# Kernel tuning notes

Measured on AMD Instinct MI355X. Metric: run time of the kernel, lower is better.

The kernel has to match this reference:

```python
import jax, jax.numpy as jnp
import numpy as np

N, E, B = 50000, 800000, 64
IN, H, OUT = 64, 128, 64


def _gcn_norm(edge_index, num_nodes):
    # PyG gcn_norm with add_self_loops=True: A_hat = A + I, norm = d^-1/2[src]*d^-1/2[dst]
    loop = jnp.arange(num_nodes)
    src = jnp.concatenate([edge_index[0], loop])
    dst = jnp.concatenate([edge_index[1], loop])
    deg = jax.ops.segment_sum(jnp.ones_like(dst, dtype=jnp.float32), dst,
                              num_segments=num_nodes)  # >= 1 due to self-loops
    dis = deg ** -0.5
    norm = dis[src] * dis[dst]  # [E+N]
    return src, dst, norm


def _gcn_layer(x, W, b, src, dst, norm, num_nodes):
    h = x @ W                                   # linear first (GCNConv order)
    msg = h[src] * norm[:, None]                # gather + normalize, [E+N, H]
    out = jax.ops.segment_sum(msg, dst, num_segments=num_nodes)  # scatter-add
    return out + b


def setup_inputs() -> dict:
    key = jax.random.key(0)
    ks = jax.random.split(key, 12)
    x = jax.random.normal(ks[0], (N, IN), dtype=jnp.float32)
    edge_index = jax.random.randint(ks[1], (2, E), 0, N, dtype=jnp.int64)
    batch = jnp.sort(jax.random.randint(ks[2], (N,), 0, B, dtype=jnp.int64))

    def lin(k, fan_in, fan_out):
        s = 1.0 / np.sqrt(fan_in)
        return jax.random.uniform(k, (fan_in, fan_out), jnp.float32, -s, s)

    return {
        "x": x, "edge_index": edge_index, "batch": batch,
        "W1": lin(ks[3], IN, H), "b1": jnp.zeros((H,), jnp.float32),
        "W2": lin(ks[4], H, H),  "b2": jnp.zeros((H,), jnp.float32),
        "W3": lin(ks[5], H, H),  "b3": jnp.zeros((H,), jnp.float32),
        "W4": lin(ks[6], H, OUT), "b4": jnp.zeros((OUT,), jnp.float32),
    }


def reference(x, edge_index, batch, W1, b1, W2, b2, W3, b3, W4, b4):
    src, dst, norm = _gcn_norm(edge_index, N)
    h = jax.nn.relu(_gcn_layer(x, W1, b1, src, dst, norm, N))
    h = jax.nn.relu(_gcn_layer(h, W2, b2, src, dst, norm, N))
    # global mean pool over graphs
    sums = jax.ops.segment_sum(h, batch, num_segments=B)          # [B, H]
    cnts = jax.ops.segment_sum(jnp.ones((N,), jnp.float32), batch, num_segments=B)
    pooled = sums / jnp.maximum(cnts, 1.0)[:, None]
    # MLP head
    return jax.nn.relu(pooled @ W3 + b3) @ W4 + b4                # [B, OUT]
```

## Files before the change

kernel.cpp:

```cpp
#include <hip/hip_runtime.h>


__device__ __forceinline__ float ldf(const void* p, long long i, int f32) {
    if (f32) return ((const float*)p)[i];
    unsigned int u = ((const unsigned short*)p)[i];
    return __uint_as_float(u << 16);
}
__device__ __forceinline__ float bfl(unsigned int u) { return __uint_as_float(u << 16); }
__device__ __forceinline__ float bfh(unsigned int u) { return __uint_as_float(u & 0xFFFF0000u); }
__device__ __forceinline__ int ld_idx(const int* p, long long i, int i64) {
    return i64 ? p[2 * i] : p[i];
}
__device__ __forceinline__ unsigned short f2bf(float v) {
    unsigned int x = __float_as_uint(v);
    return (unsigned short)((x + 0x7FFFu + ((x >> 16) & 1u)) >> 16);
}
__device__ __forceinline__ int clampi(int v, int lo, int hi) {
    return v < lo ? lo : (v > hi ? hi : v);
}

#define OW1 0
#define OB1 8192
#define OW2 8320
#define OB2 24704
// ... 1 lines not shown
#define OB3 41216
#define OW4 41344
#define OB4 49536
#define OTOT 49600


__global__ void gnn_prep(const void* W1, const void* b1, const void* W2, const void* b2,
                         const void* W3, const void* b3, const void* W4, const void* b4,
                         const void* x, const int* __restrict__ ei,
                         int* __restrict__ flags_out,
                         int* __restrict__ degcnt, float* __restrict__ pooled,
                         float* __restrict__ wsW, unsigned short* __restrict__ xb,
                         int N, int B) {
    __shared__ int s_cnt, s_or;
    const int t = threadIdx.x;
    if (t == 0) { s_cnt = 0; s_or = 0; }
    __syncthreads();
    {
        const unsigned int* w1w = (const unsigned int*)W1;
        int c = 0, o = 0;
        for (int i = t; i < 512; i += 256) {
            unsigned int e = (w1w[i] >> 7) & 0xFFu;
            if (e >= 100 && e <= 140) c++;
        }
        for (int i = t; i < 1024; i += 256) o |= ei[2 * i + 1];
        atomicAdd(&s_cnt, c);
        atomicOr(&s_or, o);
    }
    __syncthreads();
    const int f32 = (s_cnt > 256) ? 0 : 1;
    if (blockIdx.x == 0 && t == 0) {
        flags_out[0] = f32;
        flags_out[1] = (s_or == 0) ? 1 : 0;
    }
    const int i = blockIdx.x * 256 + t;
    const int stride = gridDim.x * 256;
    for (int j = i; j < N; j += stride) degcnt[j] = 0;
    for (int j = i; j < B * 128; j += stride) pooled[j] = 0.f;
    for (int j = i; j < OTOT; j += stride) {
        float v;
        if      (j < OB1) v = ldf(W1, j - OW1, f32);
        else if (j < OW2) v = ldf(b1, j - OB1, f32);
        else if (j < OB2) v = ldf(W2, j - OW2, f32);
        else if (j < OW3) v = ldf(b2, j - OB2, f32);
        else if (j < OB3) v = ldf(W3, j - OW3, f32);
        else if (j < OW4) v = ldf(b3, j - OB3, f32);
        else if (j < OB4) v = ldf(W4, j - OW4, f32);
        else              v = ldf(b4, j - OB4, f32);
        wsW[j] = v;
    }
    if (f32) {
        const float* xf = (const float*)x;
        for (int j = i; j < N * 64; j += stride) xb[j] = f2bf(xf[j]);
    }
}


__global__ void gnn_hist(const int* __restrict__ ei, int E, int N,
                         const int* __restrict__ flags, int* __restrict__ degcnt,
                         int* __restrict__ rank) {
    int base = (blockIdx.x * 256 + threadIdx.x) * 4;
    if (base >= E) return;
    int i64 = flags[1];
    int m = min(4, E - base);
    int d[4], r[4];
#pragma unroll
    for (int j = 0; j < 4; ++j)
        if (j < m) d[j] = clampi(ld_idx(ei, (long long)E + base + j, i64), 0, N - 1);
#pragma unroll
    for (int j = 0; j < 4; ++j)
        if (j < m) r[j] = atomicAdd(&degcnt[d[j]], 1);
#pragma unroll
    for (int j = 0; j < 4; ++j)
        if (j < m) rank[base + j] = r[j];
}

__global__ void gnn_scan1(const int* __restrict__ cnt, int* __restrict__ excl,
                          int* __restrict__ sums, float* __restrict__ dis, int N) {
    __shared__ int sh[256];
    int t = threadIdx.x;
    int i = blockIdx.x * 256 + t;
    int v = (i < N) ? cnt[i] : 0;
    sh[t] = v;
    __syncthreads();
    for (int off = 1; off < 256; off <<= 1) {
        int a = (t >= off) ? sh[t - off] : 0;
        __syncthreads();
        sh[t] += a;
        __syncthreads();
    }
    if (i < N) {
        excl[i] = sh[t] - v;
        dis[i] = rsqrtf((float)v + 1.0f);
    }
    if (t == 255) sums[blockIdx.x] = sh[255];
}

__global__ void gnn_scan2(int* __restrict__ sums, int nb) {
    __shared__ int sh[256];
    int t = threadIdx.x;
    int v = (t < nb) ? sums[t] : 0;
    sh[t] = v;
    __syncthreads();
    for (int off = 1; off < 256; off <<= 1) {
        int a = (t >= off) ? sh[t - off] : 0;
        __syncthreads();
        sh[t] += a;
        __syncthreads();
    }
    if (t < nb) sums[t] = sh[t] - v;
}

template <bool SMALLN>
__global__ void gnn_fill(const int* __restrict__ ei, const int* __restrict__ excl,
                         const int* __restrict__ bsums, const int* __restrict__ rank,
                         void* __restrict__ csr, int E, int N,
                         const int* __restrict__ flags) {
    int e = blockIdx.x * 256 + threadIdx.x;
    if (e >= E) return;
    int i64 = flags[1];
    int s = clampi(ld_idx(ei, (long long)e, i64), 0, N - 1);
    int d = clampi(ld_idx(ei, (long long)E + e, i64), 0, N - 1);
    int pos = excl[d] + bsums[d >> 8] + rank[e];
    if (SMALLN) ((unsigned short*)csr)[pos] = (unsigned short)s;
    else        ((int*)csr)[pos] = s;
}

template <bool SMALLN>
__device__ __forceinline__ int csr_at(const void* csr, int e) {
    return SMALLN ? (int)((const unsigned short*)csr)[e] : ((const int*)csr)[e];
}


template <bool SMALLN>
__global__ __launch_bounds__(128) void gnn_aggx_lin1(const void* __restrict__ x,
                                                     const unsigned short* __restrict__ xconv,
                                                     const int* __restrict__ excl,
                                                     const int* __restrict__ bsums,
                                                     const void* __restrict__ csr,
                                                     const float* __restrict__ dis,
                                                     const int* __restrict__ flags,
                                                     const float* __restrict__ Wf,
                                                     const float* __restrict__ bias,
                                                     int N, int E, float* __restrict__ out) {
    __shared__ float Xs[16 * 64];
    const unsigned int* tab = flags[0] ? (const unsigned int*)xconv : (const unsigned int*)x;
    const int t = threadIdx.x;
    const int nbase = blockIdx.x * 16;
    const int lane = t & 63;
    const int fl = lane & 31;

#pragma unroll
    for (int pass = 0; pass < 4; ++pass) {
        int ln = pass * 4 + (t >> 6) * 2 + (lane >> 5);
        int n = nbase + ln;
        float a0 = 0.f, a1 = 0.f;
        if (n < N) {
            float dn = dis[n], dn2 = dn * dn;
            unsigned int us = tab[(long long)n * 32 + fl];
            a0 = bfl(us) * dn2; a1 = bfh(us) * dn2;
            int beg = excl[n] + bsums[n >> 8];
            int end = (n + 1 < N) ? (excl[n + 1] + bsums[(n + 1) >> 8]) : E;
            int e = beg;
            for (; e + 8 <= end; e += 8) {
                int s0 = csr_at<SMALLN>(csr, e),     s1 = csr_at<SMALLN>(csr, e + 1);
                int s2 = csr_at<SMALLN>(csr, e + 2), s3 = csr_at<SMALLN>(csr, e + 3);
                int s4 = csr_at<SMALLN>(csr, e + 4), s5 = csr_at<SMALLN>(csr, e + 5);
                int s6 = csr_at<SMALLN>(csr, e + 6), s7 = csr_at<SMALLN>(csr, e + 7);
                float w0 = dis[s0], w1 = dis[s1], w2 = dis[s2], w3 = dis[s3];
                float w4 = dis[s4], w5 = dis[s5], w6 = dis[s6], w7 = dis[s7];
                unsigned int u0 = tab[(long long)s0 * 32 + fl];
                unsigned int u1 = tab[(long long)s1 * 32 + fl];
                unsigned int u2 = tab[(long long)s2 * 32 + fl];
                unsigned int u3 = tab[(long long)s3 * 32 + fl];
                unsigned int u4 = tab[(long long)s4 * 32 + fl];
                unsigned int u5 = tab[(long long)s5 * 32 + fl];
                unsigned int u6 = tab[(long long)s6 * 32 + fl];
// ... 36 lines not shown
    __syncthreads();

    const int fg = t & 31, ng = t >> 5;
    const int f0 = fg * 4, n0 = ng * 4;
    const float4* Xs4 = (const float4*)Xs;
    const float4* Wp  = (const float4*)Wf;
    float4 acc[4];
#pragma unroll
    for (int j = 0; j < 4; ++j) acc[j] = make_float4(0.f, 0.f, 0.f, 0.f);
#pragma unroll 4
    for (int k4 = 0; k4 < 16; ++k4) {
        const float4 wa = Wp[(4 * k4 + 0) * 32 + fg];
        const float4 wb = Wp[(4 * k4 + 1) * 32 + fg];
        const float4 wc = Wp[(4 * k4 + 2) * 32 + fg];
        const float4 wd = Wp[(4 * k4 + 3) * 32 + fg];
#pragma unroll
        for (int j = 0; j < 4; ++j) {
            const float4 xv = Xs4[(n0 + j) * 16 + k4];
            acc[j].x = fmaf(xv.x, wa.x, acc[j].x); acc[j].y = fmaf(xv.x, wa.y, acc[j].y);
            acc[j].z = fmaf(xv.x, wa.z, acc[j].z); acc[j].w = fmaf(xv.x, wa.w, acc[j].w);
            acc[j].x = fmaf(xv.y, wb.x, acc[j].x); acc[j].y = fmaf(xv.y, wb.y, acc[j].y);
            acc[j].z = fmaf(xv.y, wb.z, acc[j].z); acc[j].w = fmaf(xv.y, wb.w, acc[j].w);
            acc[j].x = fmaf(xv.z, wc.x, acc[j].x); acc[j].y = fmaf(xv.z, wc.y, acc[j].y);
            acc[j].z = fmaf(xv.z, wc.z, acc[j].z); acc[j].w = fmaf(xv.z, wc.w, acc[j].w);
            acc[j].x = fmaf(xv.w, wd.x, acc[j].x); acc[j].y = fmaf(xv.w, wd.y, acc[j].y);
            acc[j].z = fmaf(xv.w, wd.z, acc[j].z); acc[j].w = fmaf(xv.w, wd.w, acc[j].w);
        }
    }
    const float4 b = *(const float4*)&bias[f0];
#pragma unroll
    for (int j = 0; j < 4; ++j) {
        int n = nbase + n0 + j;
        if (n >= N) continue;
        float4 a = acc[j];
        a.x = fmaxf(a.x + b.x, 0.f);
        a.y = fmaxf(a.y + b.y, 0.f);
        a.z = fmaxf(a.z + b.z, 0.f);
        a.w = fmaxf(a.w + b.w, 0.f);
        *(float4*)(out + (long long)n * 128 + f0) = a;
    }
}


template <int K, bool RELU, bool OUTBF>
__global__ __launch_bounds__(128) void gnn_linear(const float* __restrict__ X,
                                                  const float* __restrict__ Wf,
                                                  const float* __restrict__ bias,
                                                  int N, void* __restrict__ out) {
    __shared__ float Xs[16 * K];
    const int t = threadIdx.x;
    const int nbase = blockIdx.x * 16;

#pragma unroll
    for (int it = 0; it < K / 32; ++it) {
        int i4 = t + it * 128;
        int n = nbase + (i4 * 4) / K;
        float4 v = make_float4(0.f, 0.f, 0.f, 0.f);
        if (n < N) v = ((const float4*)X)[(long long)nbase * (K / 4) + i4];
        ((float4*)Xs)[i4] = v;
    }
    __syncthreads();

    const int fg = t & 31, ng = t >> 5;
    const int f0 = fg * 4, n0 = ng * 4;
    const float4* Xs4 = (const float4*)Xs;
    const float4* Wp  = (const float4*)Wf;
    float4 acc[4];
#pragma unroll
    for (int j = 0; j < 4; ++j) acc[j] = make_float4(0.f, 0.f, 0.f, 0.f);
#pragma unroll 4
    for (int k4 = 0; k4 < K / 4; ++k4) {
        const float4 wa = Wp[(4 * k4 + 0) * 32 + fg];
        const float4 wb = Wp[(4 * k4 + 1) * 32 + fg];
        const float4 wc = Wp[(4 * k4 + 2) * 32 + fg];
        const float4 wd = Wp[(4 * k4 + 3) * 32 + fg];
#pragma unroll
        for (int j = 0; j < 4; ++j) {
            const float4 xv = Xs4[(n0 + j) * (K / 4) + k4];
            acc[j].x = fmaf(xv.x, wa.x, acc[j].x); acc[j].y = fmaf(xv.x, wa.y, acc[j].y);
            acc[j].z = fmaf(xv.x, wa.z, acc[j].z); acc[j].w = fmaf(xv.x, wa.w, acc[j].w);
            acc[j].x = fmaf(xv.y, wb.x, acc[j].x); acc[j].y = fmaf(xv.y, wb.y, acc[j].y);
            acc[j].z = fmaf(xv.y, wb.z, acc[j].z); acc[j].w = fmaf(xv.y, wb.w, acc[j].w);
            acc[j].x = fmaf(xv.z, wc.x, acc[j].x); acc[j].y = fmaf(xv.z, wc.y, acc[j].y);
            acc[j].z = fmaf(xv.z, wc.z, acc[j].z); acc[j].w = fmaf(xv.z, wc.w, acc[j].w);
            acc[j].x = fmaf(xv.w, wd.x, acc[j].x); acc[j].y = fmaf(xv.w, wd.y, acc[j].y);
            acc[j].z = fmaf(xv.w, wd.z, acc[j].z); acc[j].w = fmaf(xv.w, wd.w, acc[j].w);
        }
    }
#pragma unroll
    for (int j = 0; j < 4; ++j) {
        int n = nbase + n0 + j;
        if (n >= N) continue;
        float4 a = acc[j];
        if (RELU) {
            const float4 b = *(const float4*)&bias[f0];
            a.x = fmaxf(a.x + b.x, 0.f);
            a.y = fmaxf(a.y + b.y, 0.f);
            a.z = fmaxf(a.z + b.z, 0.f);
            a.w = fmaxf(a.w + b.w, 0.f);
        }
        if (OUTBF) {
            uint2 u;
            u.x = (unsigned int)f2bf(a.x) | ((unsigned int)f2bf(a.y) << 16);
            u.y = (unsigned int)f2bf(a.z) | ((unsigned int)f2bf(a.w) << 16);
            *(uint2*)((unsigned short*)out + (long long)n * 128 + f0) = u;
        } else {
            *(float4*)((float*)out + (long long)n * 128 + f0) = a;
        }
    }
}


template <bool SMALLN>
__global__ __launch_bounds__(256) void gnn_agg_bf(const unsigned short* __restrict__ A2,
                                                  const int* __restrict__ excl,
                                                  const int* __restrict__ bsums,
                                                  const void* __restrict__ csr,
                                                  const float* __restrict__ dis,
                                                  const float* __restrict__ bias,
                                                  float* __restrict__ outC, int N, int E) {
    int t = threadIdx.x;
    int lane = t & 63;
    int n = blockIdx.x * 8 + (t >> 6) * 2 + (lane >> 5);
    if (n >= N) return;
    int fl = lane & 31;
    float dn = dis[n];
    float dn2 = dn * dn;
    uint2 us = *(const uint2*)(A2 + (long long)n * 128 + fl * 4);
    float a0 = bfl(us.x) * dn2, a1 = bfh(us.x) * dn2;
    float a2 = bfl(us.y) * dn2, a3 = bfh(us.y) * dn2;
    int beg = excl[n] + bsums[n >> 8];
    int end = (n + 1 < N) ? (excl[n + 1] + bsums[(n + 1) >> 8]) : E;
    int e = beg;
    for (; e + 8 <= end; e += 8) {
        int s0 = csr_at<SMALLN>(csr, e),     s1 = csr_at<SMALLN>(csr, e + 1);
        int s2 = csr_at<SMALLN>(csr, e + 2), s3 = csr_at<SMALLN>(csr, e + 3);
        int s4 = csr_at<SMALLN>(csr, e + 4), s5 = csr_at<SMALLN>(csr, e + 5);
        int s6 = csr_at<SMALLN>(csr, e + 6), s7 = csr_at<SMALLN>(csr, e + 7);
        float w0 = dis[s0], w1 = dis[s1], w2 = dis[s2], w3 = dis[s3];
        float w4 = dis[s4], w5 = dis[s5], w6 = dis[s6], w7 = dis[s7];
        uint2 u0 = *(const uint2*)(A2 + (long long)s0 * 128 + fl * 4);
        uint2 u1 = *(const uint2*)(A2 + (long long)s1 * 128 + fl * 4);
        uint2 u2 = *(const uint2*)(A2 + (long long)s2 * 128 + fl * 4);
        uint2 u3 = *(const uint2*)(A2 + (long long)s3 * 128 + fl * 4);
        uint2 u4 = *(const uint2*)(A2 + (long long)s4 * 128 + fl * 4);
        uint2 u5 = *(const uint2*)(A2 + (long long)s5 * 128 + fl * 4);
        uint2 u6 = *(const uint2*)(A2 + (long long)s6 * 128 + fl * 4);
        uint2 u7 = *(const uint2*)(A2 + (long long)s7 * 128 + fl * 4);
        w0 *= dn; w1 *= dn; w2 *= dn; w3 *= dn;
        w4 *= dn; w5 *= dn; w6 *= dn; w7 *= dn;
        a0 = fmaf(w0, bfl(u0.x), a0); a1 = fmaf(w0, bfh(u0.x), a1);
        a2 = fmaf(w0, bfl(u0.y), a2); a3 = fmaf(w0, bfh(u0.y), a3);
        a0 = fmaf(w1, bfl(u1.x), a0); a1 = fmaf(w1, bfh(u1.x), a1);
        a2 = fmaf(w1, bfl(u1.y), a2); a3 = fmaf(w1, bfh(u1.y), a3);
        a0 = fmaf(w2, bfl(u2.x), a0); a1 = fmaf(w2, bfh(u2.x), a1);
        a2 = fmaf(w2, bfl(u2.y), a2); a3 = fmaf(w2, bfh(u2.y), a3);
        a0 = fmaf(w3, bfl(u3.x), a0); a1 = fmaf(w3, bfh(u3.x), a1);
        a2 = fmaf(w3, bfl(u3.y), a2); a3 = fmaf(w3, bfh(u3.y), a3);
        a0 = fmaf(w4, bfl(u4.x), a0); a1 = fmaf(w4, bfh(u4.x), a1);
        a2 = fmaf(w4, bfl(u4.y), a2); a3 = fmaf(w4, bfh(u4.y), a3);
        a0 = fmaf(w5, bfl(u5.x), a0); a1 = fmaf(w5, bfh(u5.x), a1);
        a2 = fmaf(w5, bfl(u5.y), a2); a3 = fmaf(w5, bfh(u5.y), a3);
        a0 = fmaf(w6, bfl(u6.x), a0); a1 = fmaf(w6, bfh(u6.x), a1);
        a2 = fmaf(w6, bfl(u6.y), a2); a3 = fmaf(w6, bfh(u6.y), a3);
        a0 = fmaf(w7, bfl(u7.x), a0); a1 = fmaf(w7, bfh(u7.x), a1);
        a2 = fmaf(w7, bfl(u7.y), a2); a3 = fmaf(w7, bfh(u7.y), a3);
    }
    for (; e + 4 <= end; e += 4) {
        int s0 = csr_at<SMALLN>(csr, e),     s1 = csr_at<SMALLN>(csr, e + 1);
        int s2 = csr_at<SMALLN>(csr, e + 2), s3 = csr_at<SMALLN>(csr, e + 3);
        float w0 = dis[s0], w1 = dis[s1], w2 = dis[s2], w3 = dis[s3];
        uint2 u0 = *(const uint2*)(A2 + (long long)s0 * 128 + fl * 4);
        uint2 u1 = *(const uint2*)(A2 + (long long)s1 * 128 + fl * 4);
        uint2 u2 = *(const uint2*)(A2 + (long long)s2 * 128 + fl * 4);
        uint2 u3 = *(const uint2*)(A2 + (long long)s3 * 128 + fl * 4);
        w0 *= dn; w1 *= dn; w2 *= dn; w3 *= dn;
        a0 = fmaf(w0, bfl(u0.x), a0); a1 = fmaf(w0, bfh(u0.x), a1);
        a2 = fmaf(w0, bfl(u0.y), a2); a3 = fmaf(w0, bfh(u0.y), a3);
        a0 = fmaf(w1, bfl(u1.x), a0); a1 = fmaf(w1, bfh(u1.x), a1);
        a2 = fmaf(w1, bfl(u1.y), a2); a3 = fmaf(w1, bfh(u1.y), a3);
        a0 = fmaf(w2, bfl(u2.x), a0); a1 = fmaf(w2, bfh(u2.x), a1);
        a2 = fmaf(w2, bfl(u2.y), a2); a3 = fmaf(w2, bfh(u2.y), a3);
        a0 = fmaf(w3, bfl(u3.x), a0); a1 = fmaf(w3, bfh(u3.x), a1);
        a2 = fmaf(w3, bfl(u3.y), a2); a3 = fmaf(w3, bfh(u3.y), a3);
    }
    for (; e < end; ++e) {
        int s = csr_at<SMALLN>(csr, e);
        float w = dis[s] * dn;
        uint2 u = *(const uint2*)(A2 + (long long)s * 128 + fl * 4);
        a0 = fmaf(w, bfl(u.x), a0); a1 = fmaf(w, bfh(u.x), a1);
        a2 = fmaf(w, bfl(u.y), a2); a3 = fmaf(w, bfh(u.y), a3);
    }
    const float4 b = *(const float4*)&bias[fl * 4];
    float4 o;
    o.x = fmaxf(a0 + b.x, 0.f);
    o.y = fmaxf(a1 + b.y, 0.f);
    o.z = fmaxf(a2 + b.z, 0.f);
    o.w = fmaxf(a3 + b.w, 0.f);
    *(float4*)(outC + (long long)n * 128 + fl * 4) = o;
}


#define PSTRIP 32
__global__ __launch_bounds__(128) void gnn_pool(const float* __restrict__ h,
                                                const int* __restrict__ batch,
                                                const int* __restrict__ flags,
                                                float* __restrict__ pooled, int N, int B) {
    int i64 = flags[1];
    int f = threadIdx.x;
    int n0 = blockIdx.x * PSTRIP;
    if (n0 >= N) return;
    int nend = min(n0 + PSTRIP, N);
    int cur = clampi(ld_idx(batch, n0, i64), 0, B - 1);
    float acc = 0.0f;
    for (int n = n0; n < nend; ++n) {
        int b = clampi(ld_idx(batch, n, i64), 0, B - 1);
        if (b != cur) {
            atomicAdd(&pooled[cur * 128 + f], acc);
            acc = 0.0f; cur = b;
        }
        acc += h[(long long)n * 128 + f];
    }
    atomicAdd(&pooled[cur * 128 + f], acc);
}


__global__ __launch_bounds__(128) void gnn_head(const float* __restrict__ pooled,
                                                const int* __restrict__ batch,
                                                const float* __restrict__ W3,
                                                const float* __restrict__ b3,
                                                const float* __restrict__ W4,
                                                const float* __restrict__ b4,
// ... 17 lines not shown
    __syncthreads();
    float acc = b3[f];
    for (int k = 0; k < 128; ++k) acc = fmaf(xs[k], W3[k * 128 + f], acc);
    rs[f] = fmaxf(acc, 0.f);
    __syncthreads();
    if (f < 64) {
        float a2 = b4[f];
        for (int k = 0; k < 128; ++k) a2 = fmaf(rs[k], W4[k * 64 + f], a2);
        if (flags[0]) ((float*)outv)[b * 64 + f] = a2;
        else          ((unsigned short*)outv)[b * 64 + f] = f2bf(a2);
    }
}


extern "C" void kernel_launch(void* const* d_in, const int* in_sizes, int n_in,
                              void* d_out, int out_size, void* d_ws, size_t ws_size,
                              hipStream_t stream) {
    const void* x  = d_in[0];
    const int* ei  = (const int*)d_in[1];
    const int* bat = (const int*)d_in[2];

    const int N = in_sizes[0] / 64;
    const int E = in_sizes[1] / 2;
    const int B = out_size / 64;
    const bool smalln = (N < 65536);

    char* p = (char*)d_ws;
    auto alloc = [&](size_t bytes) { void* q = (void*)p; p += (bytes + 255) & ~(size_t)255; return q; };
    int*   flags    = (int*)alloc(256);
    float* wsW      = (float*)alloc((size_t)OTOT * 4);
    int*   degcnt   = (int*)alloc((size_t)N * 4);
    float* dis      = (float*)alloc((size_t)N * 4);
    int*   excl     = (int*)alloc((size_t)N * 4);
    int*   bsums    = (int*)alloc(1024);
    int*   rank     = (int*)alloc((size_t)E * 4);
    void*  csr      = alloc((size_t)E * (smalln ? 2 : 4));
    unsigned short* xb = (unsigned short*)alloc((size_t)N * 64 * 2);
    float* H1       = (float*)alloc((size_t)N * 128 * 4);
    float* C2       = (float*)alloc((size_t)N * 128 * 4);
    unsigned short* A2 = (unsigned short*)alloc((size_t)N * 128 * 2);
    float* pooled   = (float*)alloc((size_t)B * 128 * 4);
    (void)ws_size; (void)n_in;

    const int nbN = (N + 255) / 256;

    gnn_prep<<<512, 256, 0, stream>>>(d_in[3], d_in[4], d_in[5], d_in[6],
                                      d_in[7], d_in[8], d_in[9], d_in[10],
                                      x, ei, flags, degcnt, pooled, wsW, xb, N, B);

    gnn_hist<<<(E + 1023) / 1024, 256, 0, stream>>>(ei, E, N, flags, degcnt, rank);
    gnn_scan1<<<nbN, 256, 0, stream>>>(degcnt, excl, bsums, dis, N);
    gnn_scan2<<<1, 256, 0, stream>>>(bsums, nbN);
    if (smalln)
        gnn_fill<true><<<(E + 255) / 256, 256, 0, stream>>>(ei, excl, bsums, rank, csr, E, N, flags);
    else
        gnn_fill<false><<<(E + 255) / 256, 256, 0, stream>>>(ei, excl, bsums, rank, csr, E, N, flags);

    const int nlin = (N + 15) / 16;
    const int nagg = (N + 7) / 8;

    if (smalln)
        gnn_aggx_lin1<true><<<nlin, 128, 0, stream>>>(x, xb, excl, bsums, csr, dis, flags,
                                                      wsW + OW1, wsW + OB1, N, E, H1);
    else
        gnn_aggx_lin1<false><<<nlin, 128, 0, stream>>>(x, xb, excl, bsums, csr, dis, flags,
                                                       wsW + OW1, wsW + OB1, N, E, H1);

    gnn_linear<128, false, true><<<nlin, 128, 0, stream>>>(H1, wsW + OW2, wsW + OB2, N, (void*)A2);
    if (smalln)
        gnn_agg_bf<true><<<nagg, 256, 0, stream>>>(A2, excl, bsums, csr, dis, wsW + OB2, C2, N, E);
    else
        gnn_agg_bf<false><<<nagg, 256, 0, stream>>>(A2, excl, bsums, csr, dis, wsW + OB2, C2, N, E);

    gnn_pool<<<(N + PSTRIP - 1) / PSTRIP, 128, 0, stream>>>(C2, bat, flags, pooled, N, B);
    gnn_head<<<B, 128, 0, stream>>>(pooled, bat, wsW + OW3, wsW + OB3,
                                    wsW + OW4, wsW + OB4, flags, d_out, N);
}
```

Baseline: 272.2 us.

## Fuse layer-2 aggregation with linear and merge scan passes via last-block pattern

Layer 2 now aggregates first on bf16 H1 (stored by the layer-1 kernel in bf16) and then applies W2 in the same kernel. This removes the separate linear kernel and the fp32 H1 round trip. The two-kernel scan is merged into one using an atomic done-counter so the last block computes the block offsets, saving a launch. The cost is that layer 2 now gathers 128-wide bf16 rows from a reordered aggregate-then-transform schedule, and H1 is quantized to bf16.

```diff
diff --git a/kernel.cpp b/kernel.cpp
--- a/kernel.cpp
+++ b/kernel.cpp
@@ -57,6 +57,7 @@
     if (blockIdx.x == 0 && t == 0) {
         flags_out[0] = f32;
         flags_out[1] = (s_or == 0) ? 1 : 0;
+        flags_out[8] = 0;
     }
     const int i = blockIdx.x * 256 + t;
     const int stride = gridDim.x * 256;
@@ -101,8 +102,11 @@
 }
 
 __global__ void gnn_scan1(const int* __restrict__ cnt, int* __restrict__ excl,
-                          int* __restrict__ sums, float* __restrict__ dis, int N) {
+                          int* __restrict__ sums, int* __restrict__ bsums,
+                          float* __restrict__ dis, int* __restrict__ done,
+                          int N, int nb) {
     __shared__ int sh[256];
+    __shared__ int isLast;
     int t = threadIdx.x;
     int i = blockIdx.x * 256 + t;
     int v = (i < N) ? cnt[i] : 0;
@@ -119,13 +123,13 @@
         dis[i] = rsqrtf((float)v + 1.0f);
     }
     if (t == 255) sums[blockIdx.x] = sh[255];
-}
-
-__global__ void gnn_scan2(int* __restrict__ sums, int nb) {
-    __shared__ int sh[256];
-    int t = threadIdx.x;
-    int v = (t < nb) ? sums[t] : 0;
-    sh[t] = v;
+    __threadfence();
+    __syncthreads();
+    if (t == 0) isLast = (atomicAdd(done, 1) == nb - 1) ? 1 : 0;
+    __syncthreads();
+    if (!isLast) return;
+    int v2 = (t < nb) ? sums[t] : 0;
+    sh[t] = v2;
     __syncthreads();
     for (int off = 1; off < 256; off <<= 1) {
         int a = (t >= off) ? sh[t - off] : 0;
@@ -133,7 +137,7 @@
         sh[t] += a;
         __syncthreads();
     }
-    if (t < nb) sums[t] = sh[t] - v;
+    if (t < nb) bsums[t] = sh[t] - v2;
 }
 
 template <bool SMALLN>
@@ -167,7 +171,8 @@
                                                      const int* __restrict__ flags,
                                                      const float* __restrict__ Wf,
                                                      const float* __restrict__ bias,
-                                                     int N, int E, float* __restrict__ out) {
+                                                     int N, int E,
+                                                     unsigned short* __restrict__ out) {
     __shared__ float Xs[16 * 64];
     const unsigned int* tab = flags[0] ? (const unsigned int*)xconv : (const unsigned int*)x;
     const int t = threadIdx.x;
@@ -270,32 +275,107 @@
     for (int j = 0; j < 4; ++j) {
         int n = nbase + n0 + j;
         if (n >= N) continue;
-        float4 a = acc[j];
-        a.x = fmaxf(a.x + b.x, 0.f);
-        a.y = fmaxf(a.y + b.y, 0.f);
-        a.z = fmaxf(a.z + b.z, 0.f);
-        a.w = fmaxf(a.w + b.w, 0.f);
-        *(float4*)(out + (long long)n * 128 + f0) = a;
-    }
-}
-
-
-template <int K, bool RELU, bool OUTBF>
-__global__ __launch_bounds__(128) void gnn_linear(const float* __restrict__ X,
-                                                  const float* __restrict__ Wf,
-                                                  const float* __restrict__ bias,
-                                                  int N, void* __restrict__ out) {
-    __shared__ float Xs[16 * K];
+        float ax = fmaxf(acc[j].x + b.x, 0.f);
+        float ay = fmaxf(acc[j].y + b.y, 0.f);
+        float az = fmaxf(acc[j].z + b.z, 0.f);
+        float aw = fmaxf(acc[j].w + b.w, 0.f);
+        uint2 u;
+        u.x = (unsigned int)f2bf(ax) | ((unsigned int)f2bf(ay) << 16);
+        u.y = (unsigned int)f2bf(az) | ((unsigned int)f2bf(aw) << 16);
+        *(uint2*)(out + (long long)n * 128 + f0) = u;
+    }
+}
+
+
+template <bool SMALLN>
+__global__ __launch_bounds__(128) void gnn_agg_lin2(const unsigned short* __restrict__ H1,
+                                                    const int* __restrict__ excl,
+                                                    const int* __restrict__ bsums,
+                                                    const void* __restrict__ csr,
+                                                    const float* __restrict__ dis,
+                                                    const float* __restrict__ Wf,
+                                                    const float* __restrict__ bias,
+                                                    int N, int E, float* __restrict__ outC) {
+    __shared__ float Xs[16 * 128];
     const int t = threadIdx.x;
     const int nbase = blockIdx.x * 16;
-
-#pragma unroll
-    for (int it = 0; it < K / 32; ++it) {
-        int i4 = t + it * 128;
-        int n = nbase + (i4 * 4) / K;
-        float4 v = make_float4(0.f, 0.f, 0.f, 0.f);
-        if (n < N) v = ((const float4*)X)[(long long)nbase * (K / 4) + i4];
-        ((float4*)Xs)[i4] = v;
+    const int lane = t & 63;
+    const int fl = lane & 31;
+
+#pragma unroll
+    for (int pass = 0; pass < 4; ++pass) {
+        int ln = pass * 4 + (t >> 6) * 2 + (lane >> 5);
+        int n = nbase + ln;
+        float a0 = 0.f, a1 = 0.f, a2 = 0.f, a3 = 0.f;
+        if (n < N) {
+            float dn = dis[n], dn2 = dn * dn;
+            uint2 us = *(const uint2*)(H1 + (long long)n * 128 + fl * 4);
+            a0 = bfl(us.x) * dn2; a1 = bfh(us.x) * dn2;
+            a2 = bfl(us.y) * dn2; a3 = bfh(us.y) * dn2;
+            int beg = excl[n] + bsums[n >> 8];
+            int end = (n + 1 < N) ? (excl[n + 1] + bsums[(n + 1) >> 8]) : E;
+            int e = beg;
+            for (; e + 8 <= end; e += 8) {
+                int s0 = csr_at<SMALLN>(csr, e),     s1 = csr_at<SMALLN>(csr, e + 1);
+                int s2 = csr_at<SMALLN>(csr, e + 2), s3 = csr_at<SMALLN>(csr, e + 3);
+                int s4 = csr_at<SMALLN>(csr, e + 4), s5 = csr_at<SMALLN>(csr, e + 5);
+                int s6 = csr_at<SMALLN>(csr, e + 6), s7 = csr_at<SMALLN>(csr, e + 7);
+                float w0 = dis[s0], w1 = dis[s1], w2 = dis[s2], w3 = dis[s3];
+                float w4 = dis[s4], w5 = dis[s5], w6 = dis[s6], w7 = dis[s7];
+                uint2 u0 = *(const uint2*)(H1 + (long long)s0 * 128 + fl * 4);
+                uint2 u1 = *(const uint2*)(H1 + (long long)s1 * 128 + fl * 4);
+                uint2 u2 = *(const uint2*)(H1 + (long long)s2 * 128 + fl * 4);
+                uint2 u3 = *(const uint2*)(H1 + (long long)s3 * 128 + fl * 4);
+                uint2 u4 = *(const uint2*)(H1 + (long long)s4 * 128 + fl * 4);
+                uint2 u5 = *(const uint2*)(H1 + (long long)s5 * 128 + fl * 4);
+                uint2 u6 = *(const uint2*)(H1 + (long long)s6 * 128 + fl * 4);
+                uint2 u7 = *(const uint2*)(H1 + (long long)s7 * 128 + fl * 4);
+                w0 *= dn; w1 *= dn; w2 *= dn; w3 *= dn;
+                w4 *= dn; w5 *= dn; w6 *= dn; w7 *= dn;
+                a0 = fmaf(w0, bfl(u0.x), a0); a1 = fmaf(w0, bfh(u0.x), a1);
+                a2 = fmaf(w0, bfl(u0.y), a2); a3 = fmaf(w0, bfh(u0.y), a3);
+                a0 = fmaf(w1, bfl(u1.x), a0); a1 = fmaf(w1, bfh(u1.x), a1);
+                a2 = fmaf(w1, bfl(u1.y), a2); a3 = fmaf(w1, bfh(u1.y), a3);
+                a0 = fmaf(w2, bfl(u2.x), a0); a1 = fmaf(w2, bfh(u2.x), a1);
+                a2 = fmaf(w2, bfl(u2.y), a2); a3 = fmaf(w2, bfh(u2.y), a3);
+                a0 = fmaf(w3, bfl(u3.x), a0); a1 = fmaf(w3, bfh(u3.x), a1);
+                a2 = fmaf(w3, bfl(u3.y), a2); a3 = fmaf(w3, bfh(u3.y), a3);
+                a0 = fmaf(w4, bfl(u4.x), a0); a1 = fmaf(w4, bfh(u4.x), a1);
+                a2 = fmaf(w4, bfl(u4.y), a2); a3 = fmaf(w4, bfh(u4.y), a3);
+                a0 = fmaf(w5, bfl(u5.x), a0); a1 = fmaf(w5, bfh(u5.x), a1);
+                a2 = fmaf(w5, bfl(u5.y), a2); a3 = fmaf(w5, bfh(u5.y), a3);
+                a0 = fmaf(w6, bfl(u6.x), a0); a1 = fmaf(w6, bfh(u6.x), a1);
+                a2 = fmaf(w6, bfl(u6.y), a2); a3 = fmaf(w6, bfh(u6.y), a3);
+                a0 = fmaf(w7, bfl(u7.x), a0); a1 = fmaf(w7, bfh(u7.x), a1);
+                a2 = fmaf(w7, bfl(u7.y), a2); a3 = fmaf(w7, bfh(u7.y), a3);
+            }
+            for (; e + 4 <= end; e += 4) {
+                int s0 = csr_at<SMALLN>(csr, e),     s1 = csr_at<SMALLN>(csr, e + 1);
+                int s2 = csr_at<SMALLN>(csr, e + 2), s3 = csr_at<SMALLN>(csr, e + 3);
+                float w0 = dis[s0], w1 = dis[s1], w2 = dis[s2], w3 = dis[s3];
+                uint2 u0 = *(const uint2*)(H1 + (long long)s0 * 128 + fl * 4);
+                uint2 u1 = *(const uint2*)(H1 + (long long)s1 * 128 + fl * 4);
+                uint2 u2 = *(const uint2*)(H1 + (long long)s2 * 128 + fl * 4);
+                uint2 u3 = *(const uint2*)(H1 + (long long)s3 * 128 + fl * 4);
+                w0 *= dn; w1 *= dn; w2 *= dn; w3 *= dn;
+                a0 = fmaf(w0, bfl(u0.x), a0); a1 = fmaf(w0, bfh(u0.x), a1);
+                a2 = fmaf(w0, bfl(u0.y), a2); a3 = fmaf(w0, bfh(u0.y), a3);
+                a0 = fmaf(w1, bfl(u1.x), a0); a1 = fmaf(w1, bfh(u1.x), a1);
+                a2 = fmaf(w1, bfl(u1.y), a2); a3 = fmaf(w1, bfh(u1.y), a3);
+                a0 = fmaf(w2, bfl(u2.x), a0); a1 = fmaf(w2, bfh(u2.x), a1);
+                a2 = fmaf(w2, bfl(u2.y), a2); a3 = fmaf(w2, bfh(u2.y), a3);
+                a0 = fmaf(w3, bfl(u3.x), a0); a1 = fmaf(w3, bfh(u3.x), a1);
+                a2 = fmaf(w3, bfl(u3.y), a2); a3 = fmaf(w3, bfh(u3.y), a3);
+            }
+            for (; e < end; ++e) {
+                int s = csr_at<SMALLN>(csr, e);
+                float w = dis[s] * dn;
+                uint2 u = *(const uint2*)(H1 + (long long)s * 128 + fl * 4);
+                a0 = fmaf(w, bfl(u.x), a0); a1 = fmaf(w, bfh(u.x), a1);
+                a2 = fmaf(w, bfl(u.y), a2); a3 = fmaf(w, bfh(u.y), a3);
+            }
+        }
+        *(float4*)&Xs[ln * 128 + fl * 4] = make_float4(a0, a1, a2, a3);
     }
     __syncthreads();
 
@@ -307,14 +387,14 @@
 #pragma unroll
     for (int j = 0; j < 4; ++j) acc[j] = make_float4(0.f, 0.f, 0.f, 0.f);
 #pragma unroll 4
-    for (int k4 = 0; k4 < K / 4; ++k4) {
+    for (int k4 = 0; k4 < 32; ++k4) {
         const float4 wa = Wp[(4 * k4 + 0) * 32 + fg];
         const float4 wb = Wp[(4 * k4 + 1) * 32 + fg];
         const float4 wc = Wp[(4 * k4 + 2) * 32 + fg];
         const float4 wd = Wp[(4 * k4 + 3) * 32 + fg];
 #pragma unroll
         for (int j = 0; j < 4; ++j) {
-            const float4 xv = Xs4[(n0 + j) * (K / 4) + k4];
+            const float4 xv = Xs4[(n0 + j) * 32 + k4];
             acc[j].x = fmaf(xv.x, wa.x, acc[j].x); acc[j].y = fmaf(xv.x, wa.y, acc[j].y);
             acc[j].z = fmaf(xv.x, wa.z, acc[j].z); acc[j].w = fmaf(xv.x, wa.w, acc[j].w);
             acc[j].x = fmaf(xv.y, wb.x, acc[j].x); acc[j].y = fmaf(xv.y, wb.y, acc[j].y);
@@ -325,117 +405,18 @@
             acc[j].z = fmaf(xv.w, wd.z, acc[j].z); acc[j].w = fmaf(xv.w, wd.w, acc[j].w);
         }
     }
+    const float4 b = *(const float4*)&bias[f0];
 #pragma unroll
     for (int j = 0; j < 4; ++j) {
         int n = nbase + n0 + j;
         if (n >= N) continue;
         float4 a = acc[j];
-        if (RELU) {
-            const float4 b = *(const float4*)&bias[f0];
-            a.x = fmaxf(a.x + b.x, 0.f);
-            a.y = fmaxf(a.y + b.y, 0.f);
-            a.z = fmaxf(a.z + b.z, 0.f);
-            a.w = fmaxf(a.w + b.w, 0.f);
-        }
-        if (OUTBF) {
-            uint2 u;
-            u.x = (unsigned int)f2bf(a.x) | ((unsigned int)f2bf(a.y) << 16);
-            u.y = (unsigned int)f2bf(a.z) | ((unsigned int)f2bf(a.w) << 16);
-            *(uint2*)((unsigned short*)out + (long long)n * 128 + f0) = u;
-        } else {
-            *(float4*)((float*)out + (long long)n * 128 + f0) = a;
-        }
-    }
-}
-
-
-template <bool SMALLN>
-__global__ __launch_bounds__(256) void gnn_agg_bf(const unsigned short* __restrict__ A2,
-                                                  const int* __restrict__ excl,
-                                                  const int* __restrict__ bsums,
-                                                  const void* __restrict__ csr,
-                                                  const float* __restrict__ dis,
-                                                  const float* __restrict__ bias,
-                                                  float* __restrict__ outC, int N, int E) {
-    int t = threadIdx.x;
-    int lane = t & 63;
-    int n = blockIdx.x * 8 + (t >> 6) * 2 + (lane >> 5);
-    if (n >= N) return;
-    int fl = lane & 31;
-    float dn = dis[n];
-    float dn2 = dn * dn;
-    uint2 us = *(const uint2*)(A2 + (long long)n * 128 + fl * 4);
-    float a0 = bfl(us.x) * dn2, a1 = bfh(us.x) * dn2;
-    float a2 = bfl(us.y) * dn2, a3 = bfh(us.y) * dn2;
-    int beg = excl[n] + bsums[n >> 8];
-    int end = (n + 1 < N) ? (excl[n + 1] + bsums[(n + 1) >> 8]) : E;
-    int e = beg;
-    for (; e + 8 <= end; e += 8) {
-        int s0 = csr_at<SMALLN>(csr, e),     s1 = csr_at<SMALLN>(csr, e + 1);
-        int s2 = csr_at<SMALLN>(csr, e + 2), s3 = csr_at<SMALLN>(csr, e + 3);
-        int s4 = csr_at<SMALLN>(csr, e + 4), s5 = csr_at<SMALLN>(csr, e + 5);
-        int s6 = csr_at<SMALLN>(csr, e + 6), s7 = csr_at<SMALLN>(csr, e + 7);
-        float w0 = dis[s0], w1 = dis[s1], w2 = dis[s2], w3 = dis[s3];
-        float w4 = dis[s4], w5 = dis[s5], w6 = dis[s6], w7 = dis[s7];
-        uint2 u0 = *(const uint2*)(A2 + (long long)s0 * 128 + fl * 4);
-        uint2 u1 = *(const uint2*)(A2 + (long long)s1 * 128 + fl * 4);
-        uint2 u2 = *(const uint2*)(A2 + (long long)s2 * 128 + fl * 4);
-        uint2 u3 = *(const uint2*)(A2 + (long long)s3 * 128 + fl * 4);
-        uint2 u4 = *(const uint2*)(A2 + (long long)s4 * 128 + fl * 4);
-        uint2 u5 = *(const uint2*)(A2 + (long long)s5 * 128 + fl * 4);
-        uint2 u6 = *(const uint2*)(A2 + (long long)s6 * 128 + fl * 4);
-        uint2 u7 = *(const uint2*)(A2 + (long long)s7 * 128 + fl * 4);
-        w0 *= dn; w1 *= dn; w2 *= dn; w3 *= dn;
-        w4 *= dn; w5 *= dn; w6 *= dn; w7 *= dn;
-        a0 = fmaf(w0, bfl(u0.x), a0); a1 = fmaf(w0, bfh(u0.x), a1);
-        a2 = fmaf(w0, bfl(u0.y), a2); a3 = fmaf(w0, bfh(u0.y), a3);
-        a0 = fmaf(w1, bfl(u1.x), a0); a1 = fmaf(w1, bfh(u1.x), a1);
-        a2 = fmaf(w1, bfl(u1.y), a2); a3 = fmaf(w1, bfh(u1.y), a3);
-        a0 = fmaf(w2, bfl(u2.x), a0); a1 = fmaf(w2, bfh(u2.x), a1);
-        a2 = fmaf(w2, bfl(u2.y), a2); a3 = fmaf(w2, bfh(u2.y), a3);
-        a0 = fmaf(w3, bfl(u3.x), a0); a1 = fmaf(w3, bfh(u3.x), a1);
-        a2 = fmaf(w3, bfl(u3.y), a2); a3 = fmaf(w3, bfh(u3.y), a3);
-        a0 = fmaf(w4, bfl(u4.x), a0); a1 = fmaf(w4, bfh(u4.x), a1);
-        a2 = fmaf(w4, bfl(u4.y), a2); a3 = fmaf(w4, bfh(u4.y), a3);
-        a0 = fmaf(w5, bfl(u5.x), a0); a1 = fmaf(w5, bfh(u5.x), a1);
-        a2 = fmaf(w5, bfl(u5.y), a2); a3 = fmaf(w5, bfh(u5.y), a3);
-        a0 = fmaf(w6, bfl(u6.x), a0); a1 = fmaf(w6, bfh(u6.x), a1);
-        a2 = fmaf(w6, bfl(u6.y), a2); a3 = fmaf(w6, bfh(u6.y), a3);
-        a0 = fmaf(w7, bfl(u7.x), a0); a1 = fmaf(w7, bfh(u7.x), a1);
-        a2 = fmaf(w7, bfl(u7.y), a2); a3 = fmaf(w7, bfh(u7.y), a3);
-    }
-    for (; e + 4 <= end; e += 4) {
-        int s0 = csr_at<SMALLN>(csr, e),     s1 = csr_at<SMALLN>(csr, e + 1);
-        int s2 = csr_at<SMALLN>(csr, e + 2), s3 = csr_at<SMALLN>(csr, e + 3);
-        float w0 = dis[s0], w1 = dis[s1], w2 = dis[s2], w3 = dis[s3];
-        uint2 u0 = *(const uint2*)(A2 + (long long)s0 * 128 + fl * 4);
-        uint2 u1 = *(const uint2*)(A2 + (long long)s1 * 128 + fl * 4);
-        uint2 u2 = *(const uint2*)(A2 + (long long)s2 * 128 + fl * 4);
-        uint2 u3 = *(const uint2*)(A2 + (long long)s3 * 128 + fl * 4);
-        w0 *= dn; w1 *= dn; w2 *= dn; w3 *= dn;
-        a0 = fmaf(w0, bfl(u0.x), a0); a1 = fmaf(w0, bfh(u0.x), a1);
-        a2 = fmaf(w0, bfl(u0.y), a2); a3 = fmaf(w0, bfh(u0.y), a3);
-        a0 = fmaf(w1, bfl(u1.x), a0); a1 = fmaf(w1, bfh(u1.x), a1);
-        a2 = fmaf(w1, bfl(u1.y), a2); a3 = fmaf(w1, bfh(u1.y), a3);
-        a0 = fmaf(w2, bfl(u2.x), a0); a1 = fmaf(w2, bfh(u2.x), a1);
-        a2 = fmaf(w2, bfl(u2.y), a2); a3 = fmaf(w2, bfh(u2.y), a3);
-        a0 = fmaf(w3, bfl(u3.x), a0); a1 = fmaf(w3, bfh(u3.x), a1);
-        a2 = fmaf(w3, bfl(u3.y), a2); a3 = fmaf(w3, bfh(u3.y), a3);
-    }
-    for (; e < end; ++e) {
-        int s = csr_at<SMALLN>(csr, e);
-        float w = dis[s] * dn;
-        uint2 u = *(const uint2*)(A2 + (long long)s * 128 + fl * 4);
-        a0 = fmaf(w, bfl(u.x), a0); a1 = fmaf(w, bfh(u.x), a1);
-        a2 = fmaf(w, bfl(u.y), a2); a3 = fmaf(w, bfh(u.y), a3);
-    }
-    const float4 b = *(const float4*)&bias[fl * 4];
-    float4 o;
-    o.x = fmaxf(a0 + b.x, 0.f);
-    o.y = fmaxf(a1 + b.y, 0.f);
-    o.z = fmaxf(a2 + b.z, 0.f);
-    o.w = fmaxf(a3 + b.w, 0.f);
-    *(float4*)(outC + (long long)n * 128 + fl * 4) = o;
+        a.x = fmaxf(a.x + b.x, 0.f);
+        a.y = fmaxf(a.y + b.y, 0.f);
+        a.z = fmaxf(a.z + b.z, 0.f);
+        a.w = fmaxf(a.w + b.w, 0.f);
+        *(float4*)(outC + (long long)n * 128 + f0) = a;
+    }
 }
 
 
@@ -519,13 +500,13 @@
     int*   degcnt   = (int*)alloc((size_t)N * 4);
     float* dis      = (float*)alloc((size_t)N * 4);
     int*   excl     = (int*)alloc((size_t)N * 4);
+    int*   sums     = (int*)alloc(1024);
     int*   bsums    = (int*)alloc(1024);
     int*   rank     = (int*)alloc((size_t)E * 4);
     void*  csr      = alloc((size_t)E * (smalln ? 2 : 4));
     unsigned short* xb = (unsigned short*)alloc((size_t)N * 64 * 2);
-    float* H1       = (float*)alloc((size_t)N * 128 * 4);
+    unsigned short* H1 = (unsigned short*)alloc((size_t)N * 128 * 2);
     float* C2       = (float*)alloc((size_t)N * 128 * 4);
-    unsigned short* A2 = (unsigned short*)alloc((size_t)N * 128 * 2);
     float* pooled   = (float*)alloc((size_t)B * 128 * 4);
     (void)ws_size; (void)n_in;
 
@@ -536,15 +517,13 @@
                                       x, ei, flags, degcnt, pooled, wsW, xb, N, B);
 
     gnn_hist<<<(E + 1023) / 1024, 256, 0, stream>>>(ei, E, N, flags, degcnt, rank);
-    gnn_scan1<<<nbN, 256, 0, stream>>>(degcnt, excl, bsums, dis, N);
-    gnn_scan2<<<1, 256, 0, stream>>>(bsums, nbN);
+    gnn_scan1<<<nbN, 256, 0, stream>>>(degcnt, excl, sums, bsums, dis, flags + 8, N, nbN);
     if (smalln)
         gnn_fill<true><<<(E + 255) / 256, 256, 0, stream>>>(ei, excl, bsums, rank, csr, E, N, flags);
     else
         gnn_fill<false><<<(E + 255) / 256, 256, 0, stream>>>(ei, excl, bsums, rank, csr, E, N, flags);
 
     const int nlin = (N + 15) / 16;
-    const int nagg = (N + 7) / 8;
 
     if (smalln)
         gnn_aggx_lin1<true><<<nlin, 128, 0, stream>>>(x, xb, excl, bsums, csr, dis, flags,
@@ -553,11 +532,12 @@
         gnn_aggx_lin1<false><<<nlin, 128, 0, stream>>>(x, xb, excl, bsums, csr, dis, flags,
                                                        wsW + OW1, wsW + OB1, N, E, H1);
 
-    gnn_linear<128, false, true><<<nlin, 128, 0, stream>>>(H1, wsW + OW2, wsW + OB2, N, (void*)A2);
     if (smalln)
-        gnn_agg_bf<true><<<nagg, 256, 0, stream>>>(A2, excl, bsums, csr, dis, wsW + OB2, C2, N, E);
+        gnn_agg_lin2<true><<<nlin, 128, 0, stream>>>(H1, excl, bsums, csr, dis,
+                                                     wsW + OW2, wsW + OB2, N, E, C2);
     else
-        gnn_agg_bf<false><<<nagg, 256, 0, stream>>>(A2, excl, bsums, csr, dis, wsW + OB2, C2, N, E);
+        gnn_agg_lin2<false><<<nlin, 128, 0, stream>>>(H1, excl, bsums, csr, dis,
+                                                      wsW + OW2, wsW + OB2, N, E, C2);
 
     gnn_pool<<<(N + PSTRIP - 1) / PSTRIP, 128, 0, stream>>>(C2, bat, flags, pooled, N, B);
     gnn_head<<<B, 128, 0, stream>>>(pooled, bat, wsW + OW3, wsW + OB3,
```

After: 276.5 us. No clear change (+1.6%).

## Split layer-2 aggregation into feature quarters and fuse scan passes

Applied to the files above, without the earlier changes.

The layer-2 aggregation kernel now has each 16-thread group handle one quarter of a node's 128 features with 4-byte loads. Blocks are ordered so the four quarter-blocks of the same node group are adjacent, which is meant to improve cache locality and spread the gather across more threads. Separately, the two-kernel block-sum scan is merged into one kernel: the last block to finish, found with an atomic counter, scans the block sums, removing one launch. The cost is four times as many CSR index and dis reads per edge, plus a threadfence and atomic in the scan.

```diff
diff --git a/kernel.cpp b/kernel.cpp
--- a/kernel.cpp
+++ b/kernel.cpp
@@ -57,6 +57,7 @@
     if (blockIdx.x == 0 && t == 0) {
         flags_out[0] = f32;
         flags_out[1] = (s_or == 0) ? 1 : 0;
+        flags_out[8] = 0;
     }
     const int i = blockIdx.x * 256 + t;
     const int stride = gridDim.x * 256;
@@ -101,8 +102,11 @@
 }
 
 __global__ void gnn_scan1(const int* __restrict__ cnt, int* __restrict__ excl,
-                          int* __restrict__ sums, float* __restrict__ dis, int N) {
+                          int* __restrict__ sums, int* __restrict__ bsums,
+                          float* __restrict__ dis, int* __restrict__ done,
+                          int N, int nb) {
     __shared__ int sh[256];
+    __shared__ int isLast;
     int t = threadIdx.x;
     int i = blockIdx.x * 256 + t;
     int v = (i < N) ? cnt[i] : 0;
@@ -119,13 +123,13 @@
         dis[i] = rsqrtf((float)v + 1.0f);
     }
     if (t == 255) sums[blockIdx.x] = sh[255];
-}
-
-__global__ void gnn_scan2(int* __restrict__ sums, int nb) {
-    __shared__ int sh[256];
-    int t = threadIdx.x;
-    int v = (t < nb) ? sums[t] : 0;
-    sh[t] = v;
+    __threadfence();
+    __syncthreads();
+    if (t == 0) isLast = (atomicAdd(done, 1) == nb - 1) ? 1 : 0;
+    __syncthreads();
+    if (!isLast) return;
+    int v2 = (t < nb) ? sums[t] : 0;
+    sh[t] = v2;
     __syncthreads();
     for (int off = 1; off < 256; off <<= 1) {
         int a = (t >= off) ? sh[t - off] : 0;
@@ -133,7 +137,7 @@
         sh[t] += a;
         __syncthreads();
     }
-    if (t < nb) sums[t] = sh[t] - v;
+    if (t < nb) bsums[t] = sh[t] - v2;
 }
 
 template <bool SMALLN>
@@ -350,23 +354,24 @@
 
 
 template <bool SMALLN>
-__global__ __launch_bounds__(256) void gnn_agg_bf(const unsigned short* __restrict__ A2,
-                                                  const int* __restrict__ excl,
-                                                  const int* __restrict__ bsums,
-                                                  const void* __restrict__ csr,
-                                                  const float* __restrict__ dis,
-                                                  const float* __restrict__ bias,
-                                                  float* __restrict__ outC, int N, int E) {
-    int t = threadIdx.x;
-    int lane = t & 63;
-    int n = blockIdx.x * 8 + (t >> 6) * 2 + (lane >> 5);
+__global__ __launch_bounds__(256) void gnn_agg_q(const unsigned short* __restrict__ A2,
+                                                 const int* __restrict__ excl,
+                                                 const int* __restrict__ bsums,
+                                                 const void* __restrict__ csr,
+                                                 const float* __restrict__ dis,
+                                                 const float* __restrict__ bias,
+                                                 float* __restrict__ outC, int N, int E) {
+    const int b = blockIdx.x;
+    const int q = (b & 7) >> 1;
+    const int g = (b >> 3) * 2 + (b & 1);
+    const int t = threadIdx.x;
+    const int n = g * 16 + (t >> 4);
     if (n >= N) return;
-    int fl = lane & 31;
+    const int fo = q * 32 + (t & 15) * 2;
     float dn = dis[n];
     float dn2 = dn * dn;
-    uint2 us = *(const uint2*)(A2 + (long long)n * 128 + fl * 4);
-    float a0 = bfl(us.x) * dn2, a1 = bfh(us.x) * dn2;
-    float a2 = bfl(us.y) * dn2, a3 = bfh(us.y) * dn2;
+    unsigned int us = *(const unsigned int*)(A2 + (long long)n * 128 + fo);
+    float a0 = bfl(us) * dn2, a1 = bfh(us) * dn2;
     int beg = excl[n] + bsums[n >> 8];
     int end = (n + 1 < N) ? (excl[n + 1] + bsums[(n + 1) >> 8]) : E;
     int e = beg;
@@ -377,65 +382,49 @@
         int s6 = csr_at<SMALLN>(csr, e + 6), s7 = csr_at<SMALLN>(csr, e + 7);
         float w0 = dis[s0], w1 = dis[s1], w2 = dis[s2], w3 = dis[s3];
         float w4 = dis[s4], w5 = dis[s5], w6 = dis[s6], w7 = dis[s7];
-        uint2 u0 = *(const uint2*)(A2 + (long long)s0 * 128 + fl * 4);
-        uint2 u1 = *(const uint2*)(A2 + (long long)s1 * 128 + fl * 4);
-        uint2 u2 = *(const uint2*)(A2 + (long long)s2 * 128 + fl * 4);
-        uint2 u3 = *(const uint2*)(A2 + (long long)s3 * 128 + fl * 4);
-        uint2 u4 = *(const uint2*)(A2 + (long long)s4 * 128 + fl * 4);
-        uint2 u5 = *(const uint2*)(A2 + (long long)s5 * 128 + fl * 4);
-        uint2 u6 = *(const uint2*)(A2 + (long long)s6 * 128 + fl * 4);
-        uint2 u7 = *(const uint2*)(A2 + (long long)s7 * 128 + fl * 4);
+        unsigned int u0 = *(const unsigned int*)(A2 + (long long)s0 * 128 + fo);
+        unsigned int u1 = *(const unsigned int*)(A2 + (long long)s1 * 128 + fo);
+        unsigned int u2 = *(const unsigned int*)(A2 + (long long)s2 * 128 + fo);
+        unsigned int u3 = *(const unsigned int*)(A2 + (long long)s3 * 128 + fo);
+        unsigned int u4 = *(const unsigned int*)(A2 + (long long)s4 * 128 + fo);
+        unsigned int u5 = *(const unsigned int*)(A2 + (long long)s5 * 128 + fo);
+        unsigned int u6 = *(const unsigned int*)(A2 + (long long)s6 * 128 + fo);
+        unsigned int u7 = *(const unsigned int*)(A2 + (long long)s7 * 128 + fo);
         w0 *= dn; w1 *= dn; w2 *= dn; w3 *= dn;
         w4 *= dn; w5 *= dn; w6 *= dn; w7 *= dn;
-        a0 = fmaf(w0, bfl(u0.x), a0); a1 = fmaf(w0, bfh(u0.x), a1);
-        a2 = fmaf(w0, bfl(u0.y), a2); a3 = fmaf(w0, bfh(u0.y), a3);
-        a0 = fmaf(w1, bfl(u1.x), a0); a1 = fmaf(w1, bfh(u1.x), a1);
-        a2 = fmaf(w1, bfl(u1.y), a2); a3 = fmaf(w1, bfh(u1.y), a3);
-        a0 = fmaf(w2, bfl(u2.x), a0); a1 = fmaf(w2, bfh(u2.x), a1);
-        a2 = fmaf(w2, bfl(u2.y), a2); a3 = fmaf(w2, bfh(u2.y), a3);
-        a0 = fmaf(w3, bfl(u3.x), a0); a1 = fmaf(w3, bfh(u3.x), a1);
-        a2 = fmaf(w3, bfl(u3.y), a2); a3 = fmaf(w3, bfh(u3.y), a3);
-        a0 = fmaf(w4, bfl(u4.x), a0); a1 = fmaf(w4, bfh(u4.x), a1);
-        a2 = fmaf(w4, bfl(u4.y), a2); a3 = fmaf(w4, bfh(u4.y), a3);
-        a0 = fmaf(w5, bfl(u5.x), a0); a1 = fmaf(w5, bfh(u5.x), a1);
-        a2 = fmaf(w5, bfl(u5.y), a2); a3 = fmaf(w5, bfh(u5.y), a3);
-        a0 = fmaf(w6, bfl(u6.x), a0); a1 = fmaf(w6, bfh(u6.x), a1);
-        a2 = fmaf(w6, bfl(u6.y), a2); a3 = fmaf(w6, bfh(u6.y), a3);
-        a0 = fmaf(w7, bfl(u7.x), a0); a1 = fmaf(w7, bfh(u7.x), a1);
-        a2 = fmaf(w7, bfl(u7.y), a2); a3 = fmaf(w7, bfh(u7.y), a3);
+        a0 = fmaf(w0, bfl(u0), a0); a1 = fmaf(w0, bfh(u0), a1);
+        a0 = fmaf(w1, bfl(u1), a0); a1 = fmaf(w1, bfh(u1), a1);
+        a0 = fmaf(w2, bfl(u2), a0); a1 = fmaf(w2, bfh(u2), a1);
+        a0 = fmaf(w3, bfl(u3), a0); a1 = fmaf(w3, bfh(u3), a1);
+        a0 = fmaf(w4, bfl(u4), a0); a1 = fmaf(w4, bfh(u4), a1);
+        a0 = fmaf(w5, bfl(u5), a0); a1 = fmaf(w5, bfh(u5), a1);
+        a0 = fmaf(w6, bfl(u6), a0); a1 = fmaf(w6, bfh(u6), a1);
+        a0 = fmaf(w7, bfl(u7), a0); a1 = fmaf(w7, bfh(u7), a1);
     }
     for (; e + 4 <= end; e += 4) {
         int s0 = csr_at<SMALLN>(csr, e),     s1 = csr_at<SMALLN>(csr, e + 1);
         int s2 = csr_at<SMALLN>(csr, e + 2), s3 = csr_at<SMALLN>(csr, e + 3);
         float w0 = dis[s0], w1 = dis[s1], w2 = dis[s2], w3 = dis[s3];
-        uint2 u0 = *(const uint2*)(A2 + (long long)s0 * 128 + fl * 4);
-        uint2 u1 = *(const uint2*)(A2 + (long long)s1 * 128 + fl * 4);
-        uint2 u2 = *(const uint2*)(A2 + (long long)s2 * 128 + fl * 4);
-        uint2 u3 = *(const uint2*)(A2 + (long long)s3 * 128 + fl * 4);
+        unsigned int u0 = *(const unsigned int*)(A2 + (long long)s0 * 128 + fo);
+        unsigned int u1 = *(const unsigned int*)(A2 + (long long)s1 * 128 + fo);
+        unsigned int u2 = *(const unsigned int*)(A2 + (long long)s2 * 128 + fo);
+        unsigned int u3 = *(const unsigned int*)(A2 + (long long)s3 * 128 + fo);
         w0 *= dn; w1 *= dn; w2 *= dn; w3 *= dn;
-        a0 = fmaf(w0, bfl(u0.x), a0); a1 = fmaf(w0, bfh(u0.x), a1);
-        a2 = fmaf(w0, bfl(u0.y), a2); a3 = fmaf(w0, bfh(u0.y), a3);
-        a0 = fmaf(w1, bfl(u1.x), a0); a1 = fmaf(w1, bfh(u1.x), a1);
-        a2 = fmaf(w1, bfl(u1.y), a2); a3 = fmaf(w1, bfh(u1.y), a3);
-        a0 = fmaf(w2, bfl(u2.x), a0); a1 = fmaf(w2, bfh(u2.x), a1);
-        a2 = fmaf(w2, bfl(u2.y), a2); a3 = fmaf(w2, bfh(u2.y), a3);
-        a0 = fmaf(w3, bfl(u3.x), a0); a1 = fmaf(w3, bfh(u3.x), a1);
-        a2 = fmaf(w3, bfl(u3.y), a2); a3 = fmaf(w3, bfh(u3.y), a3);
+        a0 = fmaf(w0, bfl(u0), a0); a1 = fmaf(w0, bfh(u0), a1);
+        a0 = fmaf(w1, bfl(u1), a0); a1 = fmaf(w1, bfh(u1), a1);
+        a0 = fmaf(w2, bfl(u2), a0); a1 = fmaf(w2, bfh(u2), a1);
+        a0 = fmaf(w3, bfl(u3), a0); a1 = fmaf(w3, bfh(u3), a1);
     }
     for (; e < end; ++e) {
         int s = csr_at<SMALLN>(csr, e);
         float w = dis[s] * dn;
-        uint2 u = *(const uint2*)(A2 + (long long)s * 128 + fl * 4);
-        a0 = fmaf(w, bfl(u.x), a0); a1 = fmaf(w, bfh(u.x), a1);
-        a2 = fmaf(w, bfl(u.y), a2); a3 = fmaf(w, bfh(u.y), a3);
-    }
-    const float4 b = *(const float4*)&bias[fl * 4];
-    float4 o;
-    o.x = fmaxf(a0 + b.x, 0.f);
-    o.y = fmaxf(a1 + b.y, 0.f);
-    o.z = fmaxf(a2 + b.z, 0.f);
-    o.w = fmaxf(a3 + b.w, 0.f);
-    *(float4*)(outC + (long long)n * 128 + fl * 4) = o;
+        unsigned int u = *(const unsigned int*)(A2 + (long long)s * 128 + fo);
+        a0 = fmaf(w, bfl(u), a0); a1 = fmaf(w, bfh(u), a1);
+    }
+    float2 o;
+    o.x = fmaxf(a0 + bias[fo], 0.f);
+    o.y = fmaxf(a1 + bias[fo + 1], 0.f);
+    *(float2*)(outC + (long long)n * 128 + fo) = o;
 }
 
 
@@ -519,6 +508,7 @@
     int*   degcnt   = (int*)alloc((size_t)N * 4);
     float* dis      = (float*)alloc((size_t)N * 4);
     int*   excl     = (int*)alloc((size_t)N * 4);
+    int*   sums     = (int*)alloc(1024);
     int*   bsums    = (int*)alloc(1024);
     int*   rank     = (int*)alloc((size_t)E * 4);
     void*  csr      = alloc((size_t)E * (smalln ? 2 : 4));
@@ -536,15 +526,13 @@
                                       x, ei, flags, degcnt, pooled, wsW, xb, N, B);
 
     gnn_hist<<<(E + 1023) / 1024, 256, 0, stream>>>(ei, E, N, flags, degcnt, rank);
-    gnn_scan1<<<nbN, 256, 0, stream>>>(degcnt, excl, bsums, dis, N);
-    gnn_scan2<<<1, 256, 0, stream>>>(bsums, nbN);
+    gnn_scan1<<<nbN, 256, 0, stream>>>(degcnt, excl, sums, bsums, dis, flags + 8, N, nbN);
     if (smalln)
         gnn_fill<true><<<(E + 255) / 256, 256, 0, stream>>>(ei, excl, bsums, rank, csr, E, N, flags);
     else
         gnn_fill<false><<<(E + 255) / 256, 256, 0, stream>>>(ei, excl, bsums, rank, csr, E, N, flags);
 
     const int nlin = (N + 15) / 16;
-    const int nagg = (N + 7) / 8;
 
     if (smalln)
         gnn_aggx_lin1<true><<<nlin, 128, 0, stream>>>(x, xb, excl, bsums, csr, dis, flags,
@@ -554,10 +542,12 @@
                                                        wsW + OW1, wsW + OB1, N, E, H1);
 
     gnn_linear<128, false, true><<<nlin, 128, 0, stream>>>(H1, wsW + OW2, wsW + OB2, N, (void*)A2);
+    const int nb8 = ((nlin ) + 1) / 2;
+    const int naggq = nb8 * 8;
     if (smalln)
-        gnn_agg_bf<true><<<nagg, 256, 0, stream>>>(A2, excl, bsums, csr, dis, wsW + OB2, C2, N, E);
+        gnn_agg_q<true><<<naggq, 256, 0, stream>>>(A2, excl, bsums, csr, dis, wsW + OB2, C2, N, E);
     else
-        gnn_agg_bf<false><<<nagg, 256, 0, stream>>>(A2, excl, bsums, csr, dis, wsW + OB2, C2, N, E);
+        gnn_agg_q<false><<<naggq, 256, 0, stream>>>(A2, excl, bsums, csr, dis, wsW + OB2, C2, N, E);
 
     gnn_pool<<<(N + PSTRIP - 1) / PSTRIP, 128, 0, stream>>>(C2, bat, flags, pooled, N, B);
     gnn_head<<<B, 128, 0, stream>>>(pooled, bat, wsW + OW3, wsW + OB3,
```

Result: slower. 305.9 us (+12.4%).
